# Kernel optimization log

Hardware: AMD Instinct MI355X
Metric: run time of the kernel (lower is better)

## Reference

```python
import jax, jax.numpy as jnp
import numpy as np
from jax import lax

# ---- module config (init_kwargs) ----
B, CIN, COUT, H, W, K = 16, 32, 32, 256, 256, 3
FEATURE_BITS = 8
INPUT_ZP = 3
OUTPUT_ZP = -5
INPUT_SCALE = 0.02
OUTPUT_SCALE = 0.05
STRIDE = (1, 1)
PAD_H, PAD_W = 1, 1
DILATION = (1, 1)
GROUPS = 1
QMIN, QMAX = -(2 ** (FEATURE_BITS - 1)), 2 ** (FEATURE_BITS - 1) - 1  # -128, 127


def float_to_fixed_point(scale, bitwidth):
    # Represent scale (in (0,1)) as int_scale * 2^-frac_bits with int_scale <= 2^(b-1)-1.
    # Pick the largest frac_bits s.t. round(scale * 2^frac_bits) fits -> max precision.
    qmax = jnp.float32(2 ** (bitwidth - 1) - 1)
    frac_bits = jnp.floor(jnp.log2(qmax / scale)).astype(jnp.int32)
    int_scale = jnp.round(scale * jnp.exp2(frac_bits.astype(jnp.float32))).astype(jnp.int32)
    return int_scale, frac_bits


def setup_inputs() -> dict:
    key = jax.random.key(0)
    k0, k1, k2, k3 = jax.random.split(key, 4)
    x = jax.random.randint(k0, (B, CIN, H, W), -128, 128, dtype=jnp.int32).astype(jnp.int8)
    qweight = jax.random.randint(k1, (COUT, CIN, K, K), -128, 128, dtype=jnp.int32).astype(jnp.int8)
    qbias = jax.random.randint(k2, (COUT,), -1000, 1000, dtype=jnp.int32)
    weight_scale = jax.random.uniform(k3, (COUT,), jnp.float32, 1e-3, 1e-2)
    return {"x": x, "qweight": qweight, "qbias": qbias, "weight_scale": weight_scale}


def reference(x, qweight, qbias, weight_scale):
    # F.pad(qinput, (pw,pw,ph,ph), 'constant', input_zero_point) -> pad W and H dims
    xp = jnp.pad(x, ((0, 0), (0, 0), (PAD_H, PAD_H), (PAD_W, PAD_W)),
                 mode="constant", constant_values=INPUT_ZP)
    # int32 conv (no bias), VALID since input was pre-padded
    out = lax.conv_general_dilated(
        xp.astype(jnp.int32), qweight.astype(jnp.int32),
        window_strides=STRIDE, padding="VALID", rhs_dilation=DILATION,
        dimension_numbers=("NCHW", "OIHW", "NCHW"), feature_group_count=GROUPS)
    # shifted bias: qbias - sum(qweight) * input_zero_point  (per out channel)
    shifted_qbias = qbias - qweight.astype(jnp.int32).sum((1, 2, 3)) * INPUT_ZP
    out = out + shifted_qbias[None, :, None, None]
    # fixed-point requant: (out * int_scale) >> frac_bits, per channel
    folded_scale = (INPUT_SCALE * weight_scale / OUTPUT_SCALE).astype(jnp.float32)
    int_scale, frac_bits = float_to_fixed_point(folded_scale, FEATURE_BITS)
    out = jnp.right_shift(out * int_scale[None, :, None, None],
                          frac_bits[None, :, None, None])  # arithmetic shift on int32
    out = out + OUTPUT_ZP
    out = jnp.clip(out, QMIN, QMAX).astype(jnp.int8)
    return out
```

## Files before the change

### kernel.cpp

```cpp
#include <hip/hip_runtime.h>

#define B_   16
#define CIN  32
#define COUT 32
#define H_   256
#define W_   256
#define IN_ZP  3
#define OUT_ZP (-5)
#define HW (H_ * W_)
#define TH 8
#define TW 64
#define SW 72
#define SH 10

using i32x4  = __attribute__((ext_vector_type(4))) int;
using i32x16 = __attribute__((ext_vector_type(16))) int;

__global__ void qconv_prep(const int* __restrict__ qw, const int* __restrict__ qb,
                           const float* __restrict__ wscale, int* __restrict__ ws) {
    const int co  = blockIdx.x;
    const int tid = threadIdx.x;
    __shared__ int red[4];
    const int* wco = qw + co * (CIN * 9);

    int s = 0;
    for (int i = tid; i < CIN * 9; i += 256) s += wco[i];
    for (int off = 32; off; off >>= 1) s += __shfl_down(s, off, 64);
    if ((tid & 63) == 0) red[tid >> 6] = s;

    if (tid < 72) {
        int gidx = blockIdx.x * 72 + tid;
        int g    = gidx & 3;
        int lane = (gidx >> 2) & 63;
        int t    = gidx >> 8;
        int wco2 = lane & 31;
        int ci0  = 16 * (lane >> 5) + 4 * g;
        const int* base = qw + wco2 * (CIN * 9);
        int b0 = base[(ci0 + 0) * 9 + t] & 0xff;
        int b1 = base[(ci0 + 1) * 9 + t] & 0xff;
        int b2 = base[(ci0 + 2) * 9 + t] & 0xff;
        int b3 = base[(ci0 + 3) * 9 + t] & 0xff;
        ws[gidx] = b0 | (b1 << 8) | (b2 << 16) | (b3 << 24);
    }
    __syncthreads();
    if (tid == 0) {
        int wsum = red[0] + red[1] + red[2] + red[3];
        ws[2304 + co] = qb[co] - wsum * IN_ZP;
        float fs = (0.02f * wscale[co]) / 0.05f;
        float fb = floorf(log2f(127.0f / fs));
        ws[2336 + co] = (int)rintf(fs * exp2f(fb));
        ws[2368 + co] = (int)fb;
    }
}

__global__ __launch_bounds__(256) void qconv_main(const int* __restrict__ x,
                                                  const int* __restrict__ ws,
                                                  int* __restrict__ out) {
    __shared__ int smem[8][SH][SW];
    const int wt = blockIdx.x * TW;
    const int ht = blockIdx.y * TH;
    const int b  = blockIdx.z;
    const int tid = threadIdx.x;
    const int* xb = x + b * (CIN * HW);

    for (int idx = tid; idx < 8 * SH * (SW / 4); idx += 256) {
        int cig = idx / (SH * 18);
        int rem = idx % (SH * 18);
        int r = rem / 18, c4 = rem % 18;
        int gh  = ht - 1 + r;
        int gw0 = wt - 4 + c4 * 4;
        int pk[4];
        if ((unsigned)gh < H_ && gw0 >= 0 && gw0 + 3 < W_) {
            const int* p = xb + (cig * 4) * HW + gh * W_ + gw0;
            i32x4 v0 = *(const i32x4*)(p);
            i32x4 v1 = *(const i32x4*)(p + HW);
            i32x4 v2 = *(const i32x4*)(p + 2 * HW);
            i32x4 v3 = *(const i32x4*)(p + 3 * HW);
#pragma unroll
            for (int j = 0; j < 4; ++j)
                pk[j] = (v0[j] & 0xff) | ((v1[j] & 0xff) << 8) |
                        ((v2[j] & 0xff) << 16) | (v3[j] << 24);
        } else {
#pragma unroll
            for (int j = 0; j < 4; ++j) {
                int gw = gw0 + j;
                int b0 = 3, b1 = 3, b2 = 3, b3 = 3;
                if ((unsigned)gh < H_ && (unsigned)gw < W_) {
                    const int* p = xb + (cig * 4) * HW + gh * W_ + gw;
                    b0 = p[0] & 0xff; b1 = p[HW] & 0xff;
                    b2 = p[2 * HW] & 0xff; b3 = p[3 * HW] & 0xff;
                }
                pk[j] = b0 | (b1 << 8) | (b2 << 16) | (b3 << 24);
            }
        }
#pragma unroll
        for (int j = 0; j < 4; ++j) smem[cig][r][c4 * 4 + j] = pk[j];
    }
    __syncthreads();

    const int lane = tid & 63;
    const int wv   = tid >> 6;
    const int co   = lane & 31;
    const int hh   = lane >> 5;

    i32x4 bfrag[9];
    const i32x4* bws = (const i32x4*)ws;
#pragma unroll
    for (int t = 0; t < 9; ++t) bfrag[t] = bws[t * 64 + lane];

    const int sb  = ws[2304 + co];
    const int isc = ws[2336 + co];
    const int fb  = ws[2368 + co];

#pragma unroll
    for (int i = 0; i < 4; ++i) {
        int mt = wv * 4 + i;
        int r0 = mt >> 1, chunk = mt & 1;
        i32x16 acc;
#pragma unroll
        for (int r = 0; r < 16; ++r) acc[r] = sb;
#pragma unroll
        for (int t = 0; t < 9; ++t) {
            int dh = t / 3, dw = t % 3;
            int rr = r0 + dh;
            int c  = chunk * 32 + (lane & 31) + dw + 3;
            i32x4 a;
#pragma unroll
            for (int g = 0; g < 4; ++g) a[g] = smem[4 * hh + g][rr][c];
            acc = __builtin_amdgcn_mfma_i32_32x32x32_i8(a, bfrag[t], acc, 0, 0, 0);
        }
        int* op = out + (b * COUT + co) * HW + (ht + r0) * W_ + wt + chunk * 32 + 4 * hh;
#pragma unroll
        for (int rg = 0; rg < 4; ++rg) {
            i32x4 v;
#pragma unroll
            for (int j = 0; j < 4; ++j) {
                int t2 = (int)((unsigned)acc[rg * 4 + j] * (unsigned)isc) >> fb;
                t2 += OUT_ZP;
                v[j] = min(127, max(-128, t2));
            }
            *(i32x4*)(op + 8 * rg) = v;
        }
    }
}

extern "C" void kernel_launch(void* const* d_in, const int* in_sizes, int n_in,
                              void* d_out, int out_size, void* d_ws, size_t ws_size,
                              hipStream_t stream) {
    const int*   x   = (const int*)d_in[0];
    const int*   qw  = (const int*)d_in[1];
    const int*   qb  = (const int*)d_in[2];
    const float* wsc = (const float*)d_in[3];
    int* ws  = (int*)d_ws;
    int* out = (int*)d_out;

    qconv_prep<<<32, 256, 0, stream>>>(qw, qb, wsc, ws);
    dim3 grid(W_ / TW, H_ / TH, B_);
    qconv_main<<<grid, 256, 0, stream>>>(x, ws, out);
}
```

Measured before the change: 267.2 us.

## Pre-pack int8 channels into workspace and load tiles via global_load_lds

Splits the convolution into a pack kernel that converts the int32-stored input into channel-packed 4x int8 words in workspace, followed by an MFMA kernel that reads the packed data. The MFMA kernel uses full-width 2-row tiles and fills shared memory with direct global-to-LDS loads. This removes the per-block repacking and redundant halo reads of the old kernel, but adds an extra pass that writes and then rereads a packed copy of the input. A fallback to the original kernel is kept for when the workspace is too small.

After: 257.2 us. -3.7%, faster.

```diff
diff --git a/kernel.cpp b/kernel.cpp
--- a/kernel.cpp
+++ b/kernel.cpp
@@ -8,13 +8,14 @@
 #define IN_ZP  3
 #define OUT_ZP (-5)
 #define HW (H_ * W_)
-#define TH 8
-#define TW 64
-#define SW 72
-#define SH 10
 
 using i32x4  = __attribute__((ext_vector_type(4))) int;
 using i32x16 = __attribute__((ext_vector_type(16))) int;
+
+typedef const __attribute__((address_space(1))) void* gptr_t;
+typedef __attribute__((address_space(3))) void* lptr_t;
+
+#define P8_OFF 4096
 
 __global__ void qconv_prep(const int* __restrict__ qw, const int* __restrict__ qb,
                            const float* __restrict__ wscale, int* __restrict__ ws) {
@@ -53,22 +54,119 @@
     }
 }
 
-__global__ __launch_bounds__(256) void qconv_main(const int* __restrict__ x,
+__global__ __launch_bounds__(256) void qconv_pack(const int* __restrict__ x,
+                                                  int* __restrict__ p8) {
+    int t  = blockIdx.x * 256 + threadIdx.x;
+    int w4 = t & 63;
+    int rh = t >> 6;
+    int h  = rh & 255;
+    int bc = rh >> 8;
+    const int* base = x + ((bc * 4) * H_ + h) * W_ + w4 * 4;
+    i32x4 v0 = *(const i32x4*)(base);
+    i32x4 v1 = *(const i32x4*)(base + HW);
+    i32x4 v2 = *(const i32x4*)(base + 2 * HW);
+    i32x4 v3 = *(const i32x4*)(base + 3 * HW);
+    i32x4 pk;
+#pragma unroll
+    for (int j = 0; j < 4; ++j)
+        pk[j] = (v0[j] & 0xff) | ((v1[j] & 0xff) << 8) |
+                ((v2[j] & 0xff) << 16) | (v3[j] << 24);
+    *(i32x4*)(p8 + t * 4) = pk;
+}
+
+__global__ __launch_bounds__(256) void qconv_mfma(const int* __restrict__ p8,
                                                   const int* __restrict__ ws,
                                                   int* __restrict__ out) {
+    __shared__ int smem[8][4][264];
+    const int ht   = blockIdx.x * 2;
+    const int b    = blockIdx.y;
+    const int tid  = threadIdx.x;
+    const int lane = tid & 63;
+    const int wv   = tid >> 6;
+
+#pragma unroll
+    for (int i = 0; i < 8; ++i) {
+        int idx = wv * 8 + i;
+        int cig = idx >> 2, r = idx & 3;
+        int gh  = ht - 1 + r;
+        if ((unsigned)gh < (unsigned)H_) {
+            const int* gsrc = p8 + ((b * 8 + cig) * H_ + gh) * W_ + lane * 4;
+            __builtin_amdgcn_global_load_lds((gptr_t)gsrc,
+                                             (lptr_t)&smem[cig][r][4 + lane * 4],
+                                             16, 0, 0);
+        } else {
+#pragma unroll
+            for (int k = 0; k < 4; ++k) smem[cig][r][4 + lane + 64 * k] = 0x03030303;
+        }
+    }
+    if (tid < 64) {
+        int cig = tid >> 3, r = (tid >> 1) & 3;
+        smem[cig][r][(tid & 1) ? 260 : 3] = 0x03030303;
+    }
+    __syncthreads();
+
+    const int co = lane & 31;
+    const int hh = lane >> 5;
+
+    i32x4 bfrag[9];
+    const i32x4* bws = (const i32x4*)ws;
+#pragma unroll
+    for (int t = 0; t < 9; ++t) bfrag[t] = bws[t * 64 + lane];
+
+    const int sb  = ws[2304 + co];
+    const int isc = ws[2336 + co];
+    const int fb  = ws[2368 + co];
+
+#pragma unroll
+    for (int i = 0; i < 4; ++i) {
+        int mt = wv * 4 + i;
+        int r0 = mt >> 3, chunk = mt & 7;
+        i32x16 acc;
+#pragma unroll
+        for (int r = 0; r < 16; ++r) acc[r] = sb;
+#pragma unroll
+        for (int t = 0; t < 9; ++t) {
+            int dh = t / 3, dw = t % 3;
+            int rr = r0 + dh;
+            int c  = 3 + chunk * 32 + (lane & 31) + dw;
+            i32x4 a;
+#pragma unroll
+            for (int g = 0; g < 4; ++g) a[g] = smem[4 * hh + g][rr][c];
+            acc = __builtin_amdgcn_mfma_i32_32x32x32_i8(a, bfrag[t], acc, 0, 0, 0);
+        }
+        int* op = out + (b * COUT + co) * HW + (ht + r0) * W_ + chunk * 32 + 4 * hh;
+#pragma unroll
+        for (int rg = 0; rg < 4; ++rg) {
+            i32x4 v;
+#pragma unroll
+            for (int j = 0; j < 4; ++j) {
+                int t2 = (int)((unsigned)acc[rg * 4 + j] * (unsigned)isc) >> fb;
+                t2 += OUT_ZP;
+                v[j] = min(127, max(-128, t2));
+            }
+            *(i32x4*)(op + 8 * rg) = v;
+        }
+    }
+}
+
+#define TH 8
+#define TW 64
+#define SW 72
+#define SH 10
+__global__ __launch_bounds__(256) void qconv_fb(const int* __restrict__ x,
+                                                const int* __restrict__ ws,
+                                                int* __restrict__ out) {
     __shared__ int smem[8][SH][SW];
     const int wt = blockIdx.x * TW;
     const int ht = blockIdx.y * TH;
     const int b  = blockIdx.z;
     const int tid = threadIdx.x;
     const int* xb = x + b * (CIN * HW);
-
     for (int idx = tid; idx < 8 * SH * (SW / 4); idx += 256) {
         int cig = idx / (SH * 18);
         int rem = idx % (SH * 18);
         int r = rem / 18, c4 = rem % 18;
-        int gh  = ht - 1 + r;
-        int gw0 = wt - 4 + c4 * 4;
+        int gh = ht - 1 + r, gw0 = wt - 4 + c4 * 4;
         int pk[4];
         if ((unsigned)gh < H_ && gw0 >= 0 && gw0 + 3 < W_) {
             const int* p = xb + (cig * 4) * HW + gh * W_ + gw0;
@@ -97,21 +195,13 @@
         for (int j = 0; j < 4; ++j) smem[cig][r][c4 * 4 + j] = pk[j];
     }
     __syncthreads();
-
-    const int lane = tid & 63;
-    const int wv   = tid >> 6;
-    const int co   = lane & 31;
-    const int hh   = lane >> 5;
-
+    const int lane = tid & 63, wv = tid >> 6;
+    const int co = lane & 31, hh = lane >> 5;
     i32x4 bfrag[9];
     const i32x4* bws = (const i32x4*)ws;
 #pragma unroll
     for (int t = 0; t < 9; ++t) bfrag[t] = bws[t * 64 + lane];
-
-    const int sb  = ws[2304 + co];
-    const int isc = ws[2336 + co];
-    const int fb  = ws[2368 + co];
-
+    const int sb = ws[2304 + co], isc = ws[2336 + co], fb = ws[2368 + co];
 #pragma unroll
     for (int i = 0; i < 4; ++i) {
         int mt = wv * 4 + i;
@@ -155,6 +245,15 @@
     int* out = (int*)d_out;
 
     qconv_prep<<<32, 256, 0, stream>>>(qw, qb, wsc, ws);
-    dim3 grid(W_ / TW, H_ / TH, B_);
-    qconv_main<<<grid, 256, 0, stream>>>(x, ws, out);
-}
+
+    const size_t need = (size_t)P8_OFF * 4 + (size_t)B_ * 8 * HW * 4;
+    if (ws_size >= need) {
+        int* p8 = ws + P8_OFF;
+        qconv_pack<<<8192, 256, 0, stream>>>(x, p8);
+        dim3 grid(H_ / 2, B_);
+        qconv_mfma<<<grid, 256, 0, stream>>>(p8, ws, out);
+    } else {
+        dim3 grid(W_ / TW, H_ / TH, B_);
+        qconv_fb<<<grid, 256, 0, stream>>>(x, ws, out);
+    }
+}
```

## Make staging branchless and transpose outputs through LDS for coalesced stores

Applied to the files above, without the earlier changes.

The input staging loop is unrolled into branchless items that clamp their addresses, always issue vector loads, select the zero-point pad value per element, and write to LDS with one 128-bit store. The epilogue writes requantized results into a padded per-wave LDS scratch buffer. It then reads them back so that each store instruction writes 32 consecutive width positions per channel, replacing the previous strided 16-byte stores. This trades extra LDS traffic and scratch memory, which may lower occupancy, for better global write coalescing and less divergence in staging.

New measurement: 251.6 us. 1.06x faster.

```diff
diff --git a/kernel.cpp b/kernel.cpp
--- a/kernel.cpp
+++ b/kernel.cpp
@@ -53,55 +53,55 @@
     }
 }
 
-__global__ __launch_bounds__(256) void qconv_main(const int* __restrict__ x,
-                                                  const int* __restrict__ ws,
-                                                  int* __restrict__ out) {
+__device__ __forceinline__ void stage_item(int idx, int ht, int wt,
+                                           const int* __restrict__ xb,
+                                           int (*smem)[SH][SW]) {
+    int cig = idx / 180;
+    int rem = idx - cig * 180;
+    int r   = rem / 18;
+    int c4  = rem - r * 18;
+    int gh  = ht - 1 + r;
+    int gw0 = wt - 4 + c4 * 4;
+    int ghc = min(H_ - 1, max(0, gh));
+    int gwc = min(W_ - 4, max(0, gw0));
+    const int* p = xb + (cig * 4) * HW + ghc * W_ + gwc;
+    i32x4 v0 = *(const i32x4*)(p);
+    i32x4 v1 = *(const i32x4*)(p + HW);
+    i32x4 v2 = *(const i32x4*)(p + 2 * HW);
+    i32x4 v3 = *(const i32x4*)(p + 3 * HW);
+    bool vh = (unsigned)gh < (unsigned)H_;
+    i32x4 pk;
+#pragma unroll
+    for (int j = 0; j < 4; ++j) {
+        int t = (v0[j] & 0xff) | ((v1[j] & 0xff) << 8) |
+                ((v2[j] & 0xff) << 16) | (v3[j] << 24);
+        bool ok = vh && ((unsigned)(gw0 + j) < (unsigned)W_);
+        pk[j] = ok ? t : 0x03030303;
+    }
+    *(i32x4*)&smem[cig][r][c4 * 4] = pk;
+}
+
+__global__ __launch_bounds__(256) void qconv_fused(const int* __restrict__ x,
+                                                   const int* __restrict__ ws,
+                                                   int* __restrict__ out) {
     __shared__ int smem[8][SH][SW];
+    __shared__ int scr[4][33 * 32];
     const int wt = blockIdx.x * TW;
     const int ht = blockIdx.y * TH;
     const int b  = blockIdx.z;
     const int tid = threadIdx.x;
     const int* xb = x + b * (CIN * HW);
 
-    for (int idx = tid; idx < 8 * SH * (SW / 4); idx += 256) {
-        int cig = idx / (SH * 18);
-        int rem = idx % (SH * 18);
-        int r = rem / 18, c4 = rem % 18;
-        int gh  = ht - 1 + r;
-        int gw0 = wt - 4 + c4 * 4;
-        int pk[4];
-        if ((unsigned)gh < H_ && gw0 >= 0 && gw0 + 3 < W_) {
-            const int* p = xb + (cig * 4) * HW + gh * W_ + gw0;
-            i32x4 v0 = *(const i32x4*)(p);
-            i32x4 v1 = *(const i32x4*)(p + HW);
-            i32x4 v2 = *(const i32x4*)(p + 2 * HW);
-            i32x4 v3 = *(const i32x4*)(p + 3 * HW);
-#pragma unroll
-            for (int j = 0; j < 4; ++j)
-                pk[j] = (v0[j] & 0xff) | ((v1[j] & 0xff) << 8) |
-                        ((v2[j] & 0xff) << 16) | (v3[j] << 24);
-        } else {
-#pragma unroll
-            for (int j = 0; j < 4; ++j) {
-                int gw = gw0 + j;
-                int b0 = 3, b1 = 3, b2 = 3, b3 = 3;
-                if ((unsigned)gh < H_ && (unsigned)gw < W_) {
-                    const int* p = xb + (cig * 4) * HW + gh * W_ + gw;
-                    b0 = p[0] & 0xff; b1 = p[HW] & 0xff;
-                    b2 = p[2 * HW] & 0xff; b3 = p[3 * HW] & 0xff;
-                }
-                pk[j] = b0 | (b1 << 8) | (b2 << 16) | (b3 << 24);
-            }
-        }
-#pragma unroll
-        for (int j = 0; j < 4; ++j) smem[cig][r][c4 * 4 + j] = pk[j];
-    }
+    stage_item(tid,        ht, wt, xb, smem);
+    stage_item(tid + 256,  ht, wt, xb, smem);
+    stage_item(tid + 512,  ht, wt, xb, smem);
+    stage_item(tid + 768,  ht, wt, xb, smem);
+    stage_item(tid + 1024, ht, wt, xb, smem);
+    if (tid < 160) stage_item(tid + 1280, ht, wt, xb, smem);
     __syncthreads();
 
-    const int lane = tid & 63;
-    const int wv   = tid >> 6;
-    const int co   = lane & 31;
-    const int hh   = lane >> 5;
+    const int lane = tid & 63, wv = tid >> 6;
+    const int co = lane & 31, hh = lane >> 5;
 
     i32x4 bfrag[9];
     const i32x4* bws = (const i32x4*)ws;
@@ -111,6 +111,10 @@
     const int sb  = ws[2304 + co];
     const int isc = ws[2336 + co];
     const int fb  = ws[2368 + co];
+
+    int* myscr = &scr[wv][0];
+    const int w_r   = lane & 31;
+    const int cbase = lane >> 5;
 
 #pragma unroll
     for (int i = 0; i < 4; ++i) {
@@ -129,17 +133,20 @@
             for (int g = 0; g < 4; ++g) a[g] = smem[4 * hh + g][rr][c];
             acc = __builtin_amdgcn_mfma_i32_32x32x32_i8(a, bfrag[t], acc, 0, 0, 0);
         }
-        int* op = out + (b * COUT + co) * HW + (ht + r0) * W_ + wt + chunk * 32 + 4 * hh;
 #pragma unroll
-        for (int rg = 0; rg < 4; ++rg) {
-            i32x4 v;
+        for (int rg = 0; rg < 4; ++rg)
 #pragma unroll
             for (int j = 0; j < 4; ++j) {
                 int t2 = (int)((unsigned)acc[rg * 4 + j] * (unsigned)isc) >> fb;
                 t2 += OUT_ZP;
-                v[j] = min(127, max(-128, t2));
+                t2 = min(127, max(-128, t2));
+                myscr[co * 33 + (4 * hh + 8 * rg + j)] = t2;
             }
-            *(i32x4*)(op + 8 * rg) = v;
+        int* op = out + (b * COUT) * HW + (ht + r0) * W_ + wt + chunk * 32 + w_r;
+#pragma unroll
+        for (int it = 0; it < 16; ++it) {
+            int co_r = 2 * it + cbase;
+            op[co_r * HW] = myscr[co_r * 33 + w_r];
         }
     }
 }
@@ -156,5 +163,5 @@
 
     qconv_prep<<<32, 256, 0, stream>>>(qw, qb, wsc, ws);
     dim3 grid(W_ / TW, H_ / TH, B_);
-    qconv_main<<<grid, 256, 0, stream>>>(x, ws, out);
+    qconv_fused<<<grid, 256, 0, stream>>>(x, ws, out);
 }
```
